# Kernel optimization log

Measured on AMD Instinct MI355X. Metric: run time of the kernel, lower is better.

## Reference

```python
import jax, jax.numpy as jnp
import numpy as np

N_NODES = 100000


def _gcn_norm(edge_index, num_nodes):
    # add self loops
    loops = jnp.arange(num_nodes, dtype=edge_index.dtype)
    row = jnp.concatenate([edge_index[0], loops])  # source
    col = jnp.concatenate([edge_index[1], loops])  # target
    ones = jnp.ones(row.shape[0], dtype=jnp.float32)
    deg = jax.ops.segment_sum(ones, col, num_segments=num_nodes)
    dinv = jnp.where(deg > 0, jax.lax.rsqrt(deg), 0.0)
    norm = dinv[row] * dinv[col]  # [E + N]
    return row, col, norm


def reference(x, edge_index, weight, bias):
    num_nodes = x.shape[0]
    row, col, norm = _gcn_norm(edge_index, num_nodes)
    # K = 2 hops of D^-1/2 (A + I) D^-1/2 propagation
    for _ in range(2):
        msgs = x[row] * norm[:, None]                      # [E+N, F] gather
        x = jax.ops.segment_sum(msgs, col, num_segments=num_nodes)  # scatter-add
    logits = x @ weight + bias                              # [N, classes]
    return jax.nn.log_softmax(logits, axis=1)


def setup_inputs() -> dict:
    key = jax.random.key(0)
    k1, k2, k3 = jax.random.split(key, 3)
    x = jax.random.normal(k1, (N_NODES, 128), dtype=jnp.float32)
    edge_index = jax.random.randint(k2, (2, 1600000), 0, N_NODES, dtype=jnp.int64)
    weight = jax.random.normal(k3, (128, 40), dtype=jnp.float32) * (1.0 / np.sqrt(128.0))
    bias = jnp.zeros((40,), dtype=jnp.float32)
    return {"x": x, "edge_index": edge_index, "weight": weight, "bias": bias}
```

## Files before the change

### kernel.cpp

```cpp
#include <hip/hip_runtime.h>
#include <math.h>

#define NN 100000
#define F_IN 128
#define F_OUT 40
#define FH_PAD 64
#define BSHIFT 9
#define BSIZE (1 << BSHIFT)
#define NBUCK ((NN + BSIZE - 1) >> BSHIFT)
#define SCAP 12288
#define CAP 14336
#define EPB_C 16384

typedef short bf16x8 __attribute__((ext_vector_type(8)));
typedef float f32x4 __attribute__((ext_vector_type(4)));
typedef _Float16 h2 __attribute__((ext_vector_type(2)));

union U4H { uint4 u; h2 h[4]; };

__device__ __forceinline__ short f2bf(float f) {
    union { float f; unsigned u; } uf; uf.f = f;
    unsigned r = uf.u + 0x7FFF + ((uf.u >> 16) & 1);
    return (short)(r >> 16);
}

__device__ __forceinline__ unsigned pack16(float x, float y) {
    union { _Float16 h; unsigned short s; } a, b;
    a.h = (_Float16)x; b.h = (_Float16)y;
    return (unsigned)a.s | ((unsigned)b.s << 16);
}

__device__ __forceinline__ h2 shfl_xor_h2(h2 v, int m) {
    int x = __builtin_bit_cast(int, v);
    x = __shfl_xor(x, m);
    return __builtin_bit_cast(h2, x);
}

__global__ void setup_kernel(int* __restrict__ bcursor, _Float16* xs1, _Float16* xs2) {
    int t = threadIdx.x;
    if (t < NBUCK) bcursor[t] = t * SCAP;
    if (t < 32) ((unsigned*)xs1)[(size_t)NN * 32 + t] = 0u;
    else if (t < 64) ((unsigned*)xs2)[(size_t)NN * 32 + (t - 32)] = 0u;
}

__global__ void part_kernel(const int* __restrict__ row, const int* __restrict__ col,
                            int* __restrict__ bcursor, int* __restrict__ staged, int E) {
    __shared__ int h[NBUCK];
    __shared__ int cur[NBUCK];
    for (int i = threadIdx.x; i < NBUCK; i += blockDim.x) h[i] = 0;
    __syncthreads();
    int e0 = blockIdx.x * EPB_C;
    int e1 = min(e0 + EPB_C, E);
    for (int e = e0 + threadIdx.x; e < e1; e += blockDim.x)
        atomicAdd(&h[col[e] >> BSHIFT], 1);
    __syncthreads();
    for (int i = threadIdx.x; i < NBUCK; i += blockDim.x)
        cur[i] = h[i] ? atomicAdd(&bcursor[i], h[i]) : 0;
    __syncthreads();
    for (int e = e0 + threadIdx.x; e < e1; e += blockDim.x) {
        int c = col[e];
        int pos = atomicAdd(&cur[c >> BSHIFT], 1);
        staged[pos] = ((c & (BSIZE - 1)) << 17) | row[e];
    }
}

__global__ void __launch_bounds__(512) build_kernel(const int* __restrict__ staged,
                                                    const int* __restrict__ bcursor,
                                                    int* __restrict__ adj,
                                                    int* __restrict__ offs,
                                                    float* __restrict__ dinv, int N) {
    __shared__ int hist[BSIZE];
    __shared__ int cur[BSIZE];
    __shared__ int wsum[8];
    int bk = blockIdx.x;
    int node0 = bk << BSHIFT;
    int sbase = bk * SCAP;
    int send = bcursor[bk];
    int gbase = bk * CAP;
    int i = threadIdx.x;
    hist[i] = 0;
    __syncthreads();
    for (int e = sbase + i; e < send; e += 512)
        atomicAdd(&hist[staged[e] >> 17], 1);
    __syncthreads();
    int v = hist[i];
    int Lp = (v + 2) & ~1;
    int L1 = max(Lp, __shfl_xor(Lp, 1));
    int LL = max(L1, __shfl_xor(L1, 2));
    int lane = i & 63, w = i >> 6;
    int x = LL;
#pragma unroll
    for (int d = 1; d < 64; d <<= 1) {
        int y = __shfl_up(x, d, 64);
        if (lane >= d) x += y;
    }
    if (lane == 63) wsum[w] = x;
    __syncthreads();
    int wpre = 0;
    for (int k = 0; k < w; ++k) wpre += wsum[k];
    int excl = wpre + x - LL;
    int n = node0 + i;
    if (n < N) {
        offs[n] = gbase + excl;
        dinv[n] = rsqrtf((float)v + 1.0f);
        adj[gbase + excl] = n;
        for (int p = excl + 1 + v; p < excl + LL; ++p)
            adj[gbase + p] = NN;
    }
    cur[i] = excl + 1;
    __syncthreads();
    for (int e = sbase + i; e < send; e += 512) {
        int sv = staged[e];
        int pos = atomicAdd(&cur[sv >> 17], 1);
        adj[gbase + pos] = sv & 0x1FFFF;
    }
}

__global__ void __launch_bounds__(256) gemm_kernel(const float* __restrict__ x,
                                                   const float* __restrict__ w,
                                                   const float* __restrict__ dinv,
                                                   _Float16* __restrict__ xs1, int N) {
    __shared__ bf16x8 shB[3][4][64];
    int t = threadIdx.x;
    for (int idx = t; idx < 3 * 4 * 64; idx += 256) {
        int lane = idx & 63;
        int ks = (idx >> 6) & 3;
        int jt = idx >> 8;
        int j = 16 * jt + (lane & 15);
        int k0 = 32 * ks + 8 * (lane >> 4);
        bf16x8 v;
#pragma unroll
        for (int i = 0; i < 8; ++i)
            v[i] = (j < F_OUT) ? f2bf(w[(k0 + i) * F_OUT + j]) : (short)0;
        shB[jt][ks][lane] = v;
    }
    __syncthreads();
    int wave = t >> 6, lane = t & 63;
    int node0 = blockIdx.x * 64 + wave * 16;
    if (node0 >= N) return;

    const float* xrow = x + (size_t)(node0 + (lane & 15)) * F_IN + 8 * (lane >> 4);
    f32x4 acc0 = {0.f, 0.f, 0.f, 0.f};
    f32x4 acc1 = acc0, acc2 = acc0;
#pragma unroll
    for (int ks = 0; ks < 4; ++ks) {
        float4 lo = *(const float4*)(xrow + 32 * ks);
        float4 hi = *(const float4*)(xrow + 32 * ks + 4);
        bf16x8 a;
        a[0] = f2bf(lo.x); a[1] = f2bf(lo.y); a[2] = f2bf(lo.z); a[3] = f2bf(lo.w);
        a[4] = f2bf(hi.x); a[5] = f2bf(hi.y); a[6] = f2bf(hi.z); a[7] = f2bf(hi.w);
        acc0 = __builtin_amdgcn_mfma_f32_16x16x32_bf16(a, shB[0][ks][lane], acc0, 0, 0, 0);
        acc1 = __builtin_amdgcn_mfma_f32_16x16x32_bf16(a, shB[1][ks][lane], acc1, 0, 0, 0);
        acc2 = __builtin_amdgcn_mfma_f32_16x16x32_bf16(a, shB[2][ks][lane], acc2, 0, 0, 0);
    }
    int colj = lane & 15;
    int rbase = (lane >> 4) * 4;
#pragma unroll
    for (int r = 0; r < 4; ++r) {
        int node = node0 + rbase + r;
        float d = dinv[node];
        _Float16* dst = xs1 + (size_t)node * FH_PAD;
        dst[colj]      = (_Float16)(acc0[r] * d);
        dst[16 + colj] = (_Float16)(acc1[r] * d);
        dst[32 + colj] = (colj < 8) ? (_Float16)(acc2[r] * d) : (_Float16)0.f;
        dst[48 + colj] = (_Float16)0.f;
    }
}

template <int HOP2>
__global__ void __launch_bounds__(256) hop_kernel(const int* __restrict__ offs,
                                                  const float* __restrict__ dinv,
                                                  const int* __restrict__ adj,
                                                  const _Float16* __restrict__ xs,
                                                  _Float16* __restrict__ xs_next,
                                                  const float* __restrict__ bias,
                                                  float* __restrict__ out) {
    int t = threadIdx.x;
    int wave = t >> 6, lane = t & 63;
    int n0 = blockIdx.x * 16 + wave * 4;
    int node = lane >> 4;
    int slot = (lane >> 3) & 1;
    int c = lane & 7;
    int n = n0 + node;
    int obase = offs[n];
    int L = offs[n0 + 1] - offs[n0];
    int nj = L >> 1;
    const char* xsb = (const char*)xs;
    int coff = c << 4;
    int bw = (node << 4) | slot;

    h2 A0 = {0.f, 0.f}, A1 = A0, A2 = A0, A3 = A0;
#define ACC4(q) do { A0 += q.h[0]; A1 += q.h[1]; A2 += q.h[2]; A3 += q.h[3]; } while (0)

    int li = lane & 15;
    int av0 = adj[obase + li];
    int av1 = adj[obase + 16 + li];
    int r0 = __shfl(av0, bw);
    U4H curv; curv.u = *(const uint4*)(xsb + ((size_t)(unsigned)r0 << 7) + coff);
    int jg = 1;
    int jcap = min(nj, 16);
    for (; jg < jcap; ++jg) {
        int av = (jg & 8) ? av1 : av0;
        int r2 = __shfl(av, bw + ((jg & 7) << 1));
        U4H nxt; nxt.u = *(const uint4*)(xsb + ((size_t)(unsigned)r2 << 7) + coff);
        ACC4(curv);
        curv = nxt;
    }
    for (; jg < nj; ++jg) {
        if ((jg & 7) == 0) av1 = adj[obase + ((jg >> 3) << 4) + li];
        int r2 = __shfl(av1, bw + ((jg & 7) << 1));
        U4H nxt; nxt.u = *(const uint4*)(xsb + ((size_t)(unsigned)r2 << 7) + coff);
        ACC4(curv);
        curv = nxt;
    }
    ACC4(curv);

    A0 += shfl_xor_h2(A0, 8);
    A1 += shfl_xor_h2(A1, 8);
    A2 += shfl_xor_h2(A2, 8);
    A3 += shfl_xor_h2(A3, 8);

    float f0 = (float)A0[0], f1 = (float)A0[1];
    float f2 = (float)A1[0], f3 = (float)A1[1];
    float f4 = (float)A2[0], f5 = (float)A2[1];
    float f6 = (float)A3[0], f7 = (float)A3[1];

    if (!HOP2) {
        if (slot == 0) {
            float d = dinv[n];
            float dd = d * d;
            uint4 wv;
            wv.x = pack16(f0 * dd, f1 * dd);
            wv.y = pack16(f2 * dd, f3 * dd);
            wv.z = pack16(f4 * dd, f5 * dd);
            wv.w = pack16(f6 * dd, f7 * dd);
            *(uint4*)((char*)xs_next + ((size_t)n << 7) + coff) = wv;
        }
    } else {
        float d = dinv[n];
        int col0 = 8 * c;
        bool act = col0 < F_OUT;
        float4 b0 = {0.f, 0.f, 0.f, 0.f}, b1 = b0;
        if (act) {
            b0 = ((const float4*)bias)[2 * c];
            b1 = ((const float4*)bias)[2 * c + 1];
        }
        float l0 = f0 * d + b0.x, l1 = f1 * d + b0.y;
        float l2 = f2 * d + b0.z, l3 = f3 * d + b0.w;
        float l4 = f4 * d + b1.x, l5 = f5 * d + b1.y;
        float l6 = f6 * d + b1.z, l7 = f7 * d + b1.w;
        float vm = -INFINITY;
        if (act)
            vm = fmaxf(fmaxf(fmaxf(l0, l1), fmaxf(l2, l3)),
                       fmaxf(fmaxf(l4, l5), fmaxf(l6, l7)));
#pragma unroll
        for (int off = 1; off <= 4; off <<= 1) vm = fmaxf(vm, __shfl_xor(vm, off));
        const float R = 1.44269504089f;
        float ex = 0.f;
        if (act)
            ex = exp2f((l0 - vm) * R) + exp2f((l1 - vm) * R)
               + exp2f((l2 - vm) * R) + exp2f((l3 - vm) * R)
               + exp2f((l4 - vm) * R) + exp2f((l5 - vm) * R)
               + exp2f((l6 - vm) * R) + exp2f((l7 - vm) * R);
#pragma unroll
        for (int off = 1; off <= 4; off <<= 1) ex += __shfl_xor(ex, off);
        if (slot == 0 && act) {
            float ls = vm + 0.69314718056f * log2f(ex);
            float4 q0 = {l0 - ls, l1 - ls, l2 - ls, l3 - ls};
            float4 q1 = {l4 - ls, l5 - ls, l6 - ls, l7 - ls};
            float* op = out + (size_t)n * F_OUT + col0;
            *(float4*)op = q0;
            *(float4*)(op + 4) = q1;
        }
    }
#undef ACC4
}

extern "C" void kernel_launch(void* const* d_in, const int* in_sizes, int n_in,
                              void* d_out, int out_size, void* d_ws, size_t ws_size,
                              hipStream_t stream) {
    const float* x    = (const float*)d_in[0];
    const int*   eidx = (const int*)d_in[1];
    const float* w    = (const float*)d_in[2];
    const float* bias = (const float*)d_in[3];
    float* out = (float*)d_out;

    const int E = in_sizes[1] / 2;
    const int N = NN;

    char* ws = (char*)d_ws;
    int*      bcursor = (int*)ws;      ws += 256 * 4;
    int*      offs    = (int*)ws;      ws += (size_t)N * 4;
    float*    dinv    = (float*)ws;    ws += (size_t)N * 4;
    int*      adj     = (int*)ws;      ws += (size_t)NBUCK * CAP * 4;
    _Float16* xs1     = (_Float16*)ws; ws += (size_t)(N + 1) * FH_PAD * 2;
    _Float16* xs2     = (_Float16*)ws; ws += (size_t)(N + 1) * FH_PAD * 2;
    int*      staged  = (int*)ws;

    const int* row = eidx;
    const int* col = eidx + E;

    setup_kernel<<<1, 256, 0, stream>>>(bcursor, xs1, xs2);
    part_kernel<<<(E + EPB_C - 1) / EPB_C, 1024, 0, stream>>>(row, col, bcursor, staged, E);
    build_kernel<<<NBUCK, 512, 0, stream>>>(staged, bcursor, adj, offs, dinv, N);

    gemm_kernel<<<(N + 63) / 64, 256, 0, stream>>>(x, w, dinv, xs1, N);

    hop_kernel<0><<<N / 16, 256, 0, stream>>>(offs, dinv, adj, xs1, xs2, bias, out);
    hop_kernel<1><<<N / 16, 256, 0, stream>>>(offs, dinv, adj, xs2, nullptr, bias, out);
}
```

Before: 132.3 us.

## Split fp16 feature rows into 64B+16B planes and gather three neighbors per pass

The 128-byte padded fp16 feature row (40 useful halves) is split into a 64-byte plane for columns 0-31 and a separate 16-byte plane for columns 32-39, which cuts the bytes fetched per neighbour gather. The hop kernel now uses 15 of 16 lanes per node as 3 neighbour slots times 5 column chunks, and adjacency lists are padded to multiples of three. Lane-group reductions use arbitrary-index shuffles, and the softmax reductions now run over 5 lanes. In exchange, adjacency padding grows, one lane per node sits idle, and address computation per lane is more irregular.

```diff
diff --git a/kernel.cpp b/kernel.cpp
--- a/kernel.cpp
+++ b/kernel.cpp
@@ -4,13 +4,15 @@
 #define NN 100000
 #define F_IN 128
 #define F_OUT 40
-#define FH_PAD 64
 #define BSHIFT 9
 #define BSIZE (1 << BSHIFT)
 #define NBUCK ((NN + BSIZE - 1) >> BSHIFT)
 #define SCAP 12288
 #define CAP 14336
 #define EPB_C 16384
+#define OFFB  ((unsigned)((NN + 1) * 64))
+#define ADUM  ((unsigned)(NN * 64))
+#define XSBYTES ((size_t)8000128)
 
 typedef short bf16x8 __attribute__((ext_vector_type(8)));
 typedef float f32x4 __attribute__((ext_vector_type(4)));
@@ -30,17 +32,19 @@
     return (unsigned)a.s | ((unsigned)b.s << 16);
 }
 
-__device__ __forceinline__ h2 shfl_xor_h2(h2 v, int m) {
+__device__ __forceinline__ h2 shfl_h2(h2 v, int src) {
     int x = __builtin_bit_cast(int, v);
-    x = __shfl_xor(x, m);
+    x = __shfl(x, src);
     return __builtin_bit_cast(h2, x);
 }
 
-__global__ void setup_kernel(int* __restrict__ bcursor, _Float16* xs1, _Float16* xs2) {
+__global__ void setup_kernel(int* __restrict__ bcursor, char* xs1, char* xs2) {
     int t = threadIdx.x;
     if (t < NBUCK) bcursor[t] = t * SCAP;
-    if (t < 32) ((unsigned*)xs1)[(size_t)NN * 32 + t] = 0u;
-    else if (t < 64) ((unsigned*)xs2)[(size_t)NN * 32 + (t - 32)] = 0u;
+    if (t < 16)      *(unsigned*)(xs1 + ADUM + t * 4) = 0u;
+    else if (t < 20) *(unsigned*)(xs1 + OFFB + (size_t)NN * 16 + (t - 16) * 4) = 0u;
+    else if (t < 36) *(unsigned*)(xs2 + ADUM + (t - 20) * 4) = 0u;
+    else if (t < 40) *(unsigned*)(xs2 + OFFB + (size_t)NN * 16 + (t - 36) * 4) = 0u;
 }
 
 __global__ void part_kernel(const int* __restrict__ row, const int* __restrict__ col,
@@ -84,7 +88,7 @@
         atomicAdd(&hist[staged[e] >> 17], 1);
     __syncthreads();
     int v = hist[i];
-    int Lp = (v + 2) & ~1;
+    int Lp = ((v + 3) / 3) * 3;
     int L1 = max(Lp, __shfl_xor(Lp, 1));
     int LL = max(L1, __shfl_xor(L1, 2));
     int lane = i & 63, w = i >> 6;
@@ -119,7 +123,7 @@
 __global__ void __launch_bounds__(256) gemm_kernel(const float* __restrict__ x,
                                                    const float* __restrict__ w,
                                                    const float* __restrict__ dinv,
-                                                   _Float16* __restrict__ xs1, int N) {
+                                                   char* __restrict__ xsb, int N) {
     __shared__ bf16x8 shB[3][4][64];
     int t = threadIdx.x;
     for (int idx = t; idx < 3 * 4 * 64; idx += 256) {
@@ -159,11 +163,11 @@
     for (int r = 0; r < 4; ++r) {
         int node = node0 + rbase + r;
         float d = dinv[node];
-        _Float16* dst = xs1 + (size_t)node * FH_PAD;
-        dst[colj]      = (_Float16)(acc0[r] * d);
-        dst[16 + colj] = (_Float16)(acc1[r] * d);
-        dst[32 + colj] = (colj < 8) ? (_Float16)(acc2[r] * d) : (_Float16)0.f;
-        dst[48 + colj] = (_Float16)0.f;
+        _Float16* dstA = (_Float16*)(xsb + (size_t)node * 64);
+        dstA[colj]      = (_Float16)(acc0[r] * d);
+        dstA[16 + colj] = (_Float16)(acc1[r] * d);
+        if (colj < 8)
+            ((_Float16*)(xsb + OFFB + (size_t)node * 16))[colj] = (_Float16)(acc2[r] * d);
     }
 }
 
@@ -171,54 +175,47 @@
 __global__ void __launch_bounds__(256) hop_kernel(const int* __restrict__ offs,
                                                   const float* __restrict__ dinv,
                                                   const int* __restrict__ adj,
-                                                  const _Float16* __restrict__ xs,
-                                                  _Float16* __restrict__ xs_next,
+                                                  const char* __restrict__ src,
+                                                  char* __restrict__ dst,
                                                   const float* __restrict__ bias,
                                                   float* __restrict__ out) {
     int t = threadIdx.x;
     int wave = t >> 6, lane = t & 63;
     int n0 = blockIdx.x * 16 + wave * 4;
     int node = lane >> 4;
-    int slot = (lane >> 3) & 1;
-    int c = lane & 7;
+    int sub = lane & 15;
     int n = n0 + node;
+    int s = sub / 5;
+    int q = sub - s * 5;
+    bool padl = (sub == 15);
+    unsigned strideB = padl ? 0u : (q == 4 ? 16u : 64u);
+    unsigned cstB    = padl ? ADUM : (q == 4 ? OFFB : (unsigned)(q * 16));
+
     int obase = offs[n];
     int L = offs[n0 + 1] - offs[n0];
-    int nj = L >> 1;
-    const char* xsb = (const char*)xs;
-    int coff = c << 4;
-    int bw = (node << 4) | slot;
+    int nj = L / 3;
 
     h2 A0 = {0.f, 0.f}, A1 = A0, A2 = A0, A3 = A0;
-#define ACC4(q) do { A0 += q.h[0]; A1 += q.h[1]; A2 += q.h[2]; A3 += q.h[3]; } while (0)
-
-    int li = lane & 15;
-    int av0 = adj[obase + li];
-    int av1 = adj[obase + 16 + li];
-    int r0 = __shfl(av0, bw);
-    U4H curv; curv.u = *(const uint4*)(xsb + ((size_t)(unsigned)r0 << 7) + coff);
-    int jg = 1;
-    int jcap = min(nj, 16);
-    for (; jg < jcap; ++jg) {
-        int av = (jg & 8) ? av1 : av0;
-        int r2 = __shfl(av, bw + ((jg & 7) << 1));
-        U4H nxt; nxt.u = *(const uint4*)(xsb + ((size_t)(unsigned)r2 << 7) + coff);
-        ACC4(curv);
-        curv = nxt;
-    }
-    for (; jg < nj; ++jg) {
-        if ((jg & 7) == 0) av1 = adj[obase + ((jg >> 3) << 4) + li];
-        int r2 = __shfl(av1, bw + ((jg & 7) << 1));
-        U4H nxt; nxt.u = *(const uint4*)(xsb + ((size_t)(unsigned)r2 << 7) + coff);
-        ACC4(curv);
-        curv = nxt;
-    }
-    ACC4(curv);
-
-    A0 += shfl_xor_h2(A0, 8);
-    A1 += shfl_xor_h2(A1, 8);
-    A2 += shfl_xor_h2(A2, 8);
-    A3 += shfl_xor_h2(A3, 8);
+#define ACC4(qq) do { A0 += qq.h[0]; A1 += qq.h[1]; A2 += qq.h[2]; A3 += qq.h[3]; } while (0)
+
+    int r = adj[obase + s];
+    U4H cur; cur.u = *(const uint4*)(src + (unsigned)r * strideB + cstB);
+    for (int j = 1; j < nj; ++j) {
+        int r2 = adj[obase + j * 3 + s];
+        U4H nxt; nxt.u = *(const uint4*)(src + (unsigned)r2 * strideB + cstB);
+        ACC4(cur);
+        cur = nxt;
+    }
+    ACC4(cur);
+#undef ACC4
+
+    int nb = lane & 0x30;
+    int i1 = nb | ((sub + 5) % 15);
+    int i2 = nb | ((sub + 10) % 15);
+    A0 = A0 + shfl_h2(A0, i1) + shfl_h2(A0, i2);
+    A1 = A1 + shfl_h2(A1, i1) + shfl_h2(A1, i2);
+    A2 = A2 + shfl_h2(A2, i1) + shfl_h2(A2, i2);
+    A3 = A3 + shfl_h2(A3, i1) + shfl_h2(A3, i2);
 
     float f0 = (float)A0[0], f1 = (float)A0[1];
     float f2 = (float)A1[0], f3 = (float)A1[1];
@@ -226,7 +223,7 @@
     float f6 = (float)A3[0], f7 = (float)A3[1];
 
     if (!HOP2) {
-        if (slot == 0) {
+        if (sub < 5) {
             float d = dinv[n];
             float dd = d * d;
             uint4 wv;
@@ -234,46 +231,40 @@
             wv.y = pack16(f2 * dd, f3 * dd);
             wv.z = pack16(f4 * dd, f5 * dd);
             wv.w = pack16(f6 * dd, f7 * dd);
-            *(uint4*)((char*)xs_next + ((size_t)n << 7) + coff) = wv;
+            *(uint4*)(dst + (unsigned)n * strideB + cstB) = wv;
         }
     } else {
         float d = dinv[n];
-        int col0 = 8 * c;
-        bool act = col0 < F_OUT;
-        float4 b0 = {0.f, 0.f, 0.f, 0.f}, b1 = b0;
-        if (act) {
-            b0 = ((const float4*)bias)[2 * c];
-            b1 = ((const float4*)bias)[2 * c + 1];
-        }
+        float4 b0 = ((const float4*)bias)[2 * q];
+        float4 b1 = ((const float4*)bias)[2 * q + 1];
         float l0 = f0 * d + b0.x, l1 = f1 * d + b0.y;
         float l2 = f2 * d + b0.z, l3 = f3 * d + b0.w;
         float l4 = f4 * d + b1.x, l5 = f5 * d + b1.y;
         float l6 = f6 * d + b1.z, l7 = f7 * d + b1.w;
-        float vm = -INFINITY;
-        if (act)
-            vm = fmaxf(fmaxf(fmaxf(l0, l1), fmaxf(l2, l3)),
-                       fmaxf(fmaxf(l4, l5), fmaxf(l6, l7)));
-#pragma unroll
-        for (int off = 1; off <= 4; off <<= 1) vm = fmaxf(vm, __shfl_xor(vm, off));
+        float mp = fmaxf(fmaxf(fmaxf(l0, l1), fmaxf(l2, l3)),
+                         fmaxf(fmaxf(l4, l5), fmaxf(l6, l7)));
+        float m = mp;
+#pragma unroll
+        for (int dd = 1; dd <= 4; ++dd)
+            m = fmaxf(m, __shfl(mp, nb | ((sub + dd) % 5)));
         const float R = 1.44269504089f;
-        float ex = 0.f;
-        if (act)
-            ex = exp2f((l0 - vm) * R) + exp2f((l1 - vm) * R)
-               + exp2f((l2 - vm) * R) + exp2f((l3 - vm) * R)
-               + exp2f((l4 - vm) * R) + exp2f((l5 - vm) * R)
-               + exp2f((l6 - vm) * R) + exp2f((l7 - vm) * R);
-#pragma unroll
-        for (int off = 1; off <= 4; off <<= 1) ex += __shfl_xor(ex, off);
-        if (slot == 0 && act) {
-            float ls = vm + 0.69314718056f * log2f(ex);
+        float sp = exp2f((l0 - m) * R) + exp2f((l1 - m) * R)
+                 + exp2f((l2 - m) * R) + exp2f((l3 - m) * R)
+                 + exp2f((l4 - m) * R) + exp2f((l5 - m) * R)
+                 + exp2f((l6 - m) * R) + exp2f((l7 - m) * R);
+        float sx = sp;
+#pragma unroll
+        for (int dd = 1; dd <= 4; ++dd)
+            sx += __shfl(sp, nb | ((sub + dd) % 5));
+        if (sub < 5) {
+            float ls = m + 0.69314718056f * log2f(sx);
             float4 q0 = {l0 - ls, l1 - ls, l2 - ls, l3 - ls};
             float4 q1 = {l4 - ls, l5 - ls, l6 - ls, l7 - ls};
-            float* op = out + (size_t)n * F_OUT + col0;
+            float* op = out + (size_t)n * F_OUT + 8 * q;
             *(float4*)op = q0;
             *(float4*)(op + 4) = q1;
         }
     }
-#undef ACC4
 }
 
 extern "C" void kernel_launch(void* const* d_in, const int* in_sizes, int n_in,
@@ -289,13 +280,13 @@
     const int N = NN;
 
     char* ws = (char*)d_ws;
-    int*      bcursor = (int*)ws;      ws += 256 * 4;
-    int*      offs    = (int*)ws;      ws += (size_t)N * 4;
-    float*    dinv    = (float*)ws;    ws += (size_t)N * 4;
-    int*      adj     = (int*)ws;      ws += (size_t)NBUCK * CAP * 4;
-    _Float16* xs1     = (_Float16*)ws; ws += (size_t)(N + 1) * FH_PAD * 2;
-    _Float16* xs2     = (_Float16*)ws; ws += (size_t)(N + 1) * FH_PAD * 2;
-    int*      staged  = (int*)ws;
+    int*   bcursor = (int*)ws;   ws += 256 * 4;
+    int*   offs    = (int*)ws;   ws += (size_t)N * 4;
+    float* dinv    = (float*)ws; ws += (size_t)N * 4;
+    int*   adj     = (int*)ws;   ws += (size_t)NBUCK * CAP * 4;
+    char*  xs1     = ws;         ws += XSBYTES;
+    char*  xs2     = ws;         ws += XSBYTES;
+    int*   staged  = (int*)ws;
 
     const int* row = eidx;
     const int* col = eidx + E;
```

Result: no change. 130.6 us (-1.3%).
